# Optimization experiments

Hardware: AMD Instinct MI355X
Metric: run time of the kernel (lower is better)

## Reference

```python
import jax, jax.numpy as jnp
import numpy as np

QUALITY = 50

# standard JPEG luminance / chrominance quantization tables
_Y_TABLE = np.array([
    [16, 11, 10, 16, 24, 40, 51, 61],
    [12, 12, 14, 19, 26, 58, 60, 55],
    [14, 13, 16, 24, 40, 57, 69, 56],
    [14, 17, 22, 29, 51, 87, 80, 62],
    [18, 22, 37, 56, 68, 109, 103, 77],
    [24, 35, 55, 64, 81, 104, 113, 92],
    [49, 64, 78, 87, 103, 121, 120, 101],
    [72, 92, 95, 98, 112, 100, 103, 99]], dtype=np.float32)
_C_TABLE = np.full((8, 8), 99., dtype=np.float32)
_C_TABLE[:4, :4] = np.array([[17, 18, 24, 47], [18, 21, 26, 66],
                             [24, 26, 56, 99], [47, 66, 99, 99]], dtype=np.float32)

_i = np.arange(8)
_A = np.cos((2 * _i[:, None] + 1) * _i[None, :] * np.pi / 16).astype(np.float32)
_alpha = np.array([1.0 / np.sqrt(2)] + [1.0] * 7, dtype=np.float32)
_ALPHA2 = np.outer(_alpha, _alpha).astype(np.float32)        # idct pre-scale
_SCALE = (_ALPHA2 * 0.25).astype(np.float32)                 # dct post-scale

_RGB2YCC = np.array([[0.299, 0.587, 0.114],
                     [-0.168736, -0.331264, 0.5],
                     [0.5, -0.418688, -0.081312]], dtype=np.float32)
_SHIFT1 = np.array([0., 128., 128.], dtype=np.float32)
_YCC2RGB = np.array([[1., 0., 1.402],
                     [1., -0.344136, -0.714136],
                     [1., 1.772, 0.]], dtype=np.float32)
_SHIFT2 = np.array([0., -128., -128.], dtype=np.float32)


def _diff_round(x):
    r = jnp.round(x)
    return r + (x - r) ** 3


def _jpeg_channel(ch, table, factor):
    # ch: [B, h, w] -> blockwise DCT / quantize / dequant / IDCT -> [B, h, w]
    b, h, w = ch.shape
    blocks = ch.reshape(b, h // 8, 8, w // 8, 8).transpose(0, 1, 3, 2, 4).reshape(b, -1, 8, 8)
    A = jnp.asarray(_A)
    dct = jnp.asarray(_SCALE) * jnp.einsum('bnxy,xu,yv->bnuv', blocks - 128., A, A)
    qt = jnp.asarray(table) * factor
    q = _diff_round(dct / qt)
    deq = q * qt
    idct = 0.25 * jnp.einsum('bnuv,ux,vy->bnxy', deq * jnp.asarray(_ALPHA2), A, A) + 128.
    return idct.reshape(b, h // 8, w // 8, 8, 8).transpose(0, 1, 3, 2, 4).reshape(b, h, w)


def _diff_jpeg(x, quality):
    # quality -> scaling factor
    q = float(quality)
    factor = (5000. / q if q < 50 else 200. - 2. * q) / 100.
    x = jnp.clip(x, 0., 1.)
    img = jnp.transpose(x, (0, 2, 3, 1)) * 255.                      # [B,H,W,3]
    ycc = img @ jnp.asarray(_RGB2YCC).T + jnp.asarray(_SHIFT1)
    y, cb, cr = ycc[..., 0], ycc[..., 1], ycc[..., 2]
    b, h, w = y.shape
    # 4:2:0 chroma subsampling via 2x2 average pooling
    cb_s = cb.reshape(b, h // 2, 2, w // 2, 2).mean(axis=(2, 4))
    cr_s = cr.reshape(b, h // 2, 2, w // 2, 2).mean(axis=(2, 4))
    y2 = _jpeg_channel(y, _Y_TABLE, factor)
    cb2 = _jpeg_channel(cb_s, _C_TABLE, factor)
    cr2 = _jpeg_channel(cr_s, _C_TABLE, factor)
    cb_u = jnp.repeat(jnp.repeat(cb2, 2, axis=1), 2, axis=2)
    cr_u = jnp.repeat(jnp.repeat(cr2, 2, axis=1), 2, axis=2)
    ycc2 = jnp.stack([y2, cb_u, cr_u], axis=-1)
    rgb = (ycc2 + jnp.asarray(_SHIFT2)) @ jnp.asarray(_YCC2RGB).T
    rgb = jnp.clip(rgb, 0., 255.) / 255.
    out = jnp.transpose(rgb, (0, 3, 1, 2))                           # back to NCHW
    return jnp.clip(out, 0., 1.)


def setup_inputs() -> dict:
    key = jax.random.key(0)
    x = jax.random.uniform(key, (32, 3, 512, 512), dtype=jnp.float32)
    return {"x": x}


def reference(x):
    return _diff_jpeg(x, QUALITY)
```

## Files before the change

### kernel.cpp

```cpp
#include <hip/hip_runtime.h>
#include <math.h>

#define HH 512
#define WW 512

typedef float f2 __attribute__((ext_vector_type(2)));
typedef float f4 __attribute__((ext_vector_type(4)));

#define YS2  36
#define CS2  18
#define OY   0
#define OCB  576
#define OCR  720
#define OSCR 864
#define OAB  OSCR
#define WSZ  1272

static __device__ __forceinline__ f4 vclamp01x255(f4 v) {
    f4 z = 0.f, one = 1.f;
    return __builtin_elementwise_max(__builtin_elementwise_min(v, one), z) * 255.f;
}

__device__ __constant__ float YTAB[64] = {
    16,11,10,16,24,40,51,61,
    12,12,14,19,26,58,60,55,
    14,13,16,24,40,57,69,56,
    14,17,22,29,51,87,80,62,
    18,22,37,56,68,109,103,77,
    24,35,55,64,81,104,113,92,
    49,64,78,87,103,121,120,101,
    72,92,95,98,112,100,103,99};
__device__ __constant__ float CTAB[64] = {
    17,18,24,47,99,99,99,99,
    18,21,26,66,99,99,99,99,
    24,26,56,99,99,99,99,99,
    47,66,99,99,99,99,99,99,
    99,99,99,99,99,99,99,99,
    99,99,99,99,99,99,99,99,
    99,99,99,99,99,99,99,99,
    99,99,99,99,99,99,99,99};

__global__ __launch_bounds__(256) void jpeg_fused(const float* __restrict__ in,
                                                  float* __restrict__ out)
{
#pragma clang fp contract(off)
    __shared__ float Wall[4][WSZ];

    const int tid  = threadIdx.x;
    const int wid  = tid >> 6;
    const int lane = tid & 63;
    float* W = Wall[wid];

    const int wv    = blockIdx.x * 4 + wid;
    const int b     = wv >> 9;
    const int strip = (wv >> 4) & 31;
    const int pairc = wv & 15;
    const int h0    = strip * 16;
    const int w0    = pairc * 32;
    const size_t plane = (size_t)HH * WW;

    const int rp  = lane >> 3;
    const int pr  = rp * 2;
    const int c4  = (lane & 7) * 4;
    const size_t gbase = ((size_t)b * 3 * HH + (size_t)(h0 + pr)) * WW + (w0 + c4);

    f4 Lr0 = *(const f4*)(in + gbase);
    f4 Lr1 = *(const f4*)(in + gbase + WW);
    f4 Lg0 = *(const f4*)(in + gbase + plane);
    f4 Lg1 = *(const f4*)(in + gbase + plane + WW);
    f4 Lb0 = *(const f4*)(in + gbase + 2 * plane);
    f4 Lb1 = *(const f4*)(in + gbase + 2 * plane + WW);

    {
        int x = lane >> 3, u = lane & 7;
        double arg = (double)((2 * x + 1) * u) * 3.14159265358979323846 / 16.0;
        W[OAB + lane] = (float)cos(arg);
    }
    f2 As2[32];
#pragma unroll
    for (int k = 0; k < 32; ++k) {
        As2[k][0] = __int_as_float(__builtin_amdgcn_readfirstlane(__float_as_int(W[OAB + 2 * k])));
        As2[k][1] = __int_as_float(__builtin_amdgcn_readfirstlane(__float_as_int(W[OAB + 2 * k + 1])));
    }
    asm volatile("" ::: "memory");

    {
        f4 r0 = vclamp01x255(Lr0), r1 = vclamp01x255(Lr1);
        f4 g0 = vclamp01x255(Lg0), g1 = vclamp01x255(Lg1);
        f4 b0 = vclamp01x255(Lb0), b1 = vclamp01x255(Lb1);
        f4 y0  = ((r0 * 0.299f)     + (g0 * 0.587f))     + (b0 * 0.114f);
        f4 y1  = ((r1 * 0.299f)     + (g1 * 0.587f))     + (b1 * 0.114f);
        f4 cb0 = ((r0 * -0.168736f) + (g0 * -0.331264f)) + (b0 * 0.5f);
        f4 cb1 = ((r1 * -0.168736f) + (g1 * -0.331264f)) + (b1 * 0.5f);
        f4 cr0 = ((r0 * 0.5f)       + (g0 * -0.418688f)) + (b0 * -0.081312f);
        f4 cr1 = ((r1 * 0.5f)       + (g1 * -0.418688f)) + (b1 * -0.081312f);
        cb0 = cb0 + 128.f; cb1 = cb1 + 128.f;
        cr0 = cr0 + 128.f; cr1 = cr1 + 128.f;
        y0 = y0 - 128.f;  y1 = y1 - 128.f;
        *(f4*)&W[OY + pr * YS2 + c4]       = y0;
        *(f4*)&W[OY + (pr + 1) * YS2 + c4] = y1;
        f2 mb, mr;
        {
            float s01 = cb0.x + cb0.y, s23 = cb1.x + cb1.y;
            mb[0] = (s01 + s23) / 4.0f;
            float t01 = cb0.z + cb0.w, t23 = cb1.z + cb1.w;
            mb[1] = (t01 + t23) / 4.0f;
        }
        {
            float s01 = cr0.x + cr0.y, s23 = cr1.x + cr1.y;
            mr[0] = (s01 + s23) / 4.0f;
            float t01 = cr0.z + cr0.w, t23 = cr1.z + cr1.w;
            mr[1] = (t01 + t23) / 4.0f;
        }
        *(f2*)&W[OCB + rp * CS2 + (lane & 7) * 2] = mb;
        *(f2*)&W[OCR + rp * CS2 + (lane & 7) * 2] = mr;
    }
    asm volatile("" ::: "memory");

    const int g = lane >> 3, j = lane & 7;
#pragma unroll
    for (int pass = 0; pass < 2; ++pass) {
        if (g < 6) {
            const int it   = pass * 6 + g;
            const bool isY = (it < 8);
            float* scr = &W[OSCR + g * 68];

            float X[8];
            int by = 0, bx = 0, ob = 0;
            if (isY) {
                by = it >> 2; bx = it & 3;
#pragma unroll
                for (int x = 0; x < 8; ++x)
                    X[x] = W[OY + (by * 8 + x) * YS2 + bx * 8 + j];
            } else {
                ob = (it < 10) ? OCB : OCR;
                bx = (it < 10) ? (it - 8) : (it - 10);
#pragma unroll
                for (int x = 0; x < 8; ++x)
                    X[x] = W[ob + x * CS2 + bx * 8 + j] - 128.f;
            }

            f2 Tv[4];
#pragma unroll
            for (int m = 0; m < 4; ++m) {
                f2 a = {0.f, 0.f};
#pragma unroll
                for (int x = 0; x < 8; ++x) {
                    f2 xx = {X[x], X[x]};
                    a = __builtin_elementwise_fma(xx, As2[x * 4 + m], a);
                }
                Tv[m] = a;
            }
#pragma unroll
            for (int m = 0; m < 4; ++m) {
                scr[(2 * m) * 8 + j]     = Tv[m][0];
                scr[(2 * m + 1) * 8 + j] = Tv[m][1];
            }
            float Tt[8];
            {
                float4 a = *(const float4*)&scr[j * 8];
                float4 c = *(const float4*)&scr[j * 8 + 4];
                Tt[0] = a.x; Tt[1] = a.y; Tt[2] = a.z; Tt[3] = a.w;
                Tt[4] = c.x; Tt[5] = c.y; Tt[6] = c.z; Tt[7] = c.w;
            }
            float R[8];
#pragma unroll
            for (int m = 0; m < 4; ++m) {
                f2 a = {0.f, 0.f};
#pragma unroll
                for (int y = 0; y < 8; ++y) {
                    f2 tt = {Tt[y], Tt[y]};
                    a = __builtin_elementwise_fma(tt, As2[y * 4 + m], a);
                }
                R[2 * m] = a[0]; R[2 * m + 1] = a[1];
            }
            const float* QT = isY ? YTAB : CTAB;
            float qt[8];
            {
                float4 a = *(const float4*)&QT[j * 8];
                float4 c = *(const float4*)&QT[j * 8 + 4];
                qt[0] = a.x; qt[1] = a.y; qt[2] = a.z; qt[3] = a.w;
                qt[4] = c.x; qt[5] = c.y; qt[6] = c.z; qt[7] = c.w;
            }
            const float RC = 0.70710678118654752440f;
            float au = (j == 0) ? RC : 1.0f;
            float G[8];
#pragma unroll
            for (int v = 0; v < 8; ++v) {
                float av    = (v == 0) ? RC : 1.0f;
                float a2    = au * av;
                float scale = a2 * 0.25f;
                float dct   = scale * R[v];
                float xq    = dct / qt[v];
                float rd    = rintf(xq);
                float d     = xq - rd;
                float cube  = (d * d) * d;
                float qq    = rd + cube;
                float deq   = qq * qt[v];
                G[v] = deq * a2;
            }
#pragma unroll
            for (int v = 0; v < 8; ++v) scr[v * 8 + j] = G[v];
            float Gt[8];
            {
                float4 a = *(const float4*)&scr[j * 8];
                float4 c = *(const float4*)&scr[j * 8 + 4];
                Gt[0] = a.x; Gt[1] = a.y; Gt[2] = a.z; Gt[3] = a.w;
                Gt[4] = c.x; Gt[5] = c.y; Gt[6] = c.z; Gt[7] = c.w;
            }
            f2 T2v[4];
#pragma unroll
            for (int m = 0; m < 4; ++m) {
                f2 a = {0.f, 0.f};
#pragma unroll
                for (int u = 0; u < 8; ++u) {
                    f2 gg = {Gt[u], Gt[u]};
                    a = __builtin_elementwise_fma(gg, As2[u * 4 + m], a);
                }
                T2v[m] = a;
            }
#pragma unroll
            for (int m = 0; m < 4; ++m) {
                scr[(2 * m) * 8 + j]     = T2v[m][0];
                scr[(2 * m + 1) * 8 + j] = T2v[m][1];
            }
            float T2t[8];
            {
                float4 a = *(const float4*)&scr[j * 8];
                float4 c = *(const float4*)&scr[j * 8 + 4];
                T2t[0] = a.x; T2t[1] = a.y; T2t[2] = a.z; T2t[3] = a.w;
                T2t[4] = c.x; T2t[5] = c.y; T2t[6] = c.z; T2t[7] = c.w;
            }
            float O[8];
#pragma unroll
            for (int m = 0; m < 4; ++m) {
                f2 a = {0.f, 0.f};
#pragma unroll
                for (int v = 0; v < 8; ++v) {
                    f2 tt = {T2t[v], T2t[v]};
                    a = __builtin_elementwise_fma(tt, As2[v * 4 + m], a);
                }
                a = (a * 0.25f) + 128.f;
                O[2 * m] = a[0]; O[2 * m + 1] = a[1];
            }
            if (isY) {
                *(f4*)&W[OY + (by * 8 + j) * YS2 + bx * 8]     = (f4){O[0], O[1], O[2], O[3]};
                *(f4*)&W[OY + (by * 8 + j) * YS2 + bx * 8 + 4] = (f4){O[4], O[5], O[6], O[7]};
            } else {
                *(f4*)&W[ob + j * CS2 + bx * 8]     = (f4){O[0], O[1], O[2], O[3]};
                *(f4*)&W[ob + j * CS2 + bx * 8 + 4] = (f4){O[4], O[5], O[6], O[7]};
            }
        }
        asm volatile("" ::: "memory");
    }

    {
        const float INV255 = 1.0f / 255.0f;
        f4 ya = *(const f4*)&W[OY + pr * YS2 + c4];
        f4 yb = *(const f4*)&W[OY + (pr + 1) * YS2 + c4];
        f2 cbp = *(const f2*)&W[OCB + rp * CS2 + (lane & 7) * 2];
        f2 crp = *(const f2*)&W[OCR + rp * CS2 + (lane & 7) * 2];
        float cb0 = cbp[0] - 128.f, cb1 = cbp[1] - 128.f;
        float cr0 = crp[0] - 128.f, cr1 = crp[1] - 128.f;
        f4 cbm = {cb0, cb0, cb1, cb1};
        f4 crm = {cr0, cr0, cr1, cr1};
        f4 z = 0.f, m255 = 255.f;
#pragma unroll
        for (int row = 0; row < 2; ++row) {
            f4 yy = row ? yb : ya;
            f4 rv = yy + (crm * 1.402f);
            f4 gv = (yy + (cbm * -0.344136f)) + (crm * -0.714136f);
            f4 bv = yy + (cbm * 1.772f);
            rv = __builtin_elementwise_max(__builtin_elementwise_min(rv, m255), z) * INV255;
            gv = __builtin_elementwise_max(__builtin_elementwise_min(gv, m255), z) * INV255;
            bv = __builtin_elementwise_max(__builtin_elementwise_min(bv, m255), z) * INV255;
            size_t base = gbase + (size_t)row * WW;
            __builtin_nontemporal_store(rv, (f4*)(out + base));
            __builtin_nontemporal_store(gv, (f4*)(out + base + plane));
            __builtin_nontemporal_store(bv, (f4*)(out + base + 2 * plane));
        }
    }
}

extern "C" void kernel_launch(void* const* d_in, const int* in_sizes, int n_in,
                              void* d_out, int out_size, void* d_ws, size_t ws_size,
                              hipStream_t stream)
{
    const float* x = (const float*)d_in[0];
    float* o = (float*)d_out;
    int batch  = in_sizes[0] / (3 * HH * WW);
    int blocks = batch * 512 / 4;
    jpeg_fused<<<blocks, 256, 0, stream>>>(x, o);
}
```

Measured before the change: 40.68 us.

## Process two tiles per wave with prefetch of second tile during DCT

Each wave now handles two adjacent 32-column tiles instead of one, halving the grid. The second tile's global loads are issued before the first tile's DCT work so memory latency overlaps with compute. The cosine-table setup is also amortised over two tiles. The trade-offs are higher register pressure from holding the prefetched tile and fewer waves available to hide latency.

```diff
diff --git a/kernel.cpp b/kernel.cpp
--- a/kernel.cpp
+++ b/kernel.cpp
@@ -52,42 +52,37 @@
     float* W = Wall[wid];
 
     const int wv    = blockIdx.x * 4 + wid;
-    const int b     = wv >> 9;
-    const int strip = (wv >> 4) & 31;
-    const int pairc = wv & 15;
+    const int b     = wv >> 8;
+    const int strip = (wv >> 3) & 31;
+    const int seg   = wv & 7;
     const int h0    = strip * 16;
-    const int w0    = pairc * 32;
+    const int w0    = seg * 64;
     const size_t plane = (size_t)HH * WW;
 
     const int rp  = lane >> 3;
     const int pr  = rp * 2;
     const int c4  = (lane & 7) * 4;
-    const size_t gbase = ((size_t)b * 3 * HH + (size_t)(h0 + pr)) * WW + (w0 + c4);
-
-    f4 Lr0 = *(const f4*)(in + gbase);
-    f4 Lr1 = *(const f4*)(in + gbase + WW);
-    f4 Lg0 = *(const f4*)(in + gbase + plane);
-    f4 Lg1 = *(const f4*)(in + gbase + plane + WW);
-    f4 Lb0 = *(const f4*)(in + gbase + 2 * plane);
-    f4 Lb1 = *(const f4*)(in + gbase + 2 * plane + WW);
-
-    {
-        int x = lane >> 3, u = lane & 7;
-        double arg = (double)((2 * x + 1) * u) * 3.14159265358979323846 / 16.0;
-        W[OAB + lane] = (float)cos(arg);
-    }
+    const size_t grow   = ((size_t)b * 3 * HH + (size_t)(h0 + pr)) * WW + c4;
+    const size_t gbase0 = grow + w0;
+    const size_t gbase1 = grow + w0 + 32;
+
+    const int g = lane >> 3, j = lane & 7;
     f2 As2[32];
-#pragma unroll
-    for (int k = 0; k < 32; ++k) {
-        As2[k][0] = __int_as_float(__builtin_amdgcn_readfirstlane(__float_as_int(W[OAB + 2 * k])));
-        As2[k][1] = __int_as_float(__builtin_amdgcn_readfirstlane(__float_as_int(W[OAB + 2 * k + 1])));
-    }
-    asm volatile("" ::: "memory");
-
-    {
-        f4 r0 = vclamp01x255(Lr0), r1 = vclamp01x255(Lr1);
-        f4 g0 = vclamp01x255(Lg0), g1 = vclamp01x255(Lg1);
-        f4 b0 = vclamp01x255(Lb0), b1 = vclamp01x255(Lb1);
+
+    auto loadT = [&](f4* L, size_t gb) {
+        L[0] = *(const f4*)(in + gb);
+        L[1] = *(const f4*)(in + gb + WW);
+        L[2] = *(const f4*)(in + gb + plane);
+        L[3] = *(const f4*)(in + gb + plane + WW);
+        L[4] = *(const f4*)(in + gb + 2 * plane);
+        L[5] = *(const f4*)(in + gb + 2 * plane + WW);
+    };
+
+    auto stageT = [&](const f4* L) {
+#pragma clang fp contract(off)
+        f4 r0 = vclamp01x255(L[0]), r1 = vclamp01x255(L[1]);
+        f4 g0 = vclamp01x255(L[2]), g1 = vclamp01x255(L[3]);
+        f4 b0 = vclamp01x255(L[4]), b1 = vclamp01x255(L[5]);
         f4 y0  = ((r0 * 0.299f)     + (g0 * 0.587f))     + (b0 * 0.114f);
         f4 y1  = ((r1 * 0.299f)     + (g1 * 0.587f))     + (b1 * 0.114f);
         f4 cb0 = ((r0 * -0.168736f) + (g0 * -0.331264f)) + (b0 * 0.5f);
@@ -114,147 +109,149 @@
         }
         *(f2*)&W[OCB + rp * CS2 + (lane & 7) * 2] = mb;
         *(f2*)&W[OCR + rp * CS2 + (lane & 7) * 2] = mr;
-    }
-    asm volatile("" ::: "memory");
-
-    const int g = lane >> 3, j = lane & 7;
-#pragma unroll
-    for (int pass = 0; pass < 2; ++pass) {
-        if (g < 6) {
-            const int it   = pass * 6 + g;
-            const bool isY = (it < 8);
-            float* scr = &W[OSCR + g * 68];
-
-            float X[8];
-            int by = 0, bx = 0, ob = 0;
-            if (isY) {
-                by = it >> 2; bx = it & 3;
-#pragma unroll
-                for (int x = 0; x < 8; ++x)
-                    X[x] = W[OY + (by * 8 + x) * YS2 + bx * 8 + j];
-            } else {
-                ob = (it < 10) ? OCB : OCR;
-                bx = (it < 10) ? (it - 8) : (it - 10);
-#pragma unroll
-                for (int x = 0; x < 8; ++x)
-                    X[x] = W[ob + x * CS2 + bx * 8 + j] - 128.f;
+    };
+
+    auto dctAll = [&]() {
+#pragma clang fp contract(off)
+#pragma unroll
+        for (int pass = 0; pass < 2; ++pass) {
+            if (g < 6) {
+                const int it   = pass * 6 + g;
+                const bool isY = (it < 8);
+                float* scr = &W[OSCR + g * 68];
+
+                float X[8];
+                int by = 0, bx = 0, ob = 0;
+                if (isY) {
+                    by = it >> 2; bx = it & 3;
+#pragma unroll
+                    for (int x = 0; x < 8; ++x)
+                        X[x] = W[OY + (by * 8 + x) * YS2 + bx * 8 + j];
+                } else {
+                    ob = (it < 10) ? OCB : OCR;
+                    bx = (it < 10) ? (it - 8) : (it - 10);
+#pragma unroll
+                    for (int x = 0; x < 8; ++x)
+                        X[x] = W[ob + x * CS2 + bx * 8 + j] - 128.f;
+                }
+
+                f2 Tv[4];
+#pragma unroll
+                for (int m = 0; m < 4; ++m) {
+                    f2 a = {0.f, 0.f};
+#pragma unroll
+                    for (int x = 0; x < 8; ++x) {
+                        f2 xx = {X[x], X[x]};
+                        a = __builtin_elementwise_fma(xx, As2[x * 4 + m], a);
+                    }
+                    Tv[m] = a;
+                }
+#pragma unroll
+                for (int m = 0; m < 4; ++m) {
+                    scr[(2 * m) * 8 + j]     = Tv[m][0];
+                    scr[(2 * m + 1) * 8 + j] = Tv[m][1];
+                }
+                float Tt[8];
+                {
+                    float4 a = *(const float4*)&scr[j * 8];
+                    float4 c = *(const float4*)&scr[j * 8 + 4];
+                    Tt[0] = a.x; Tt[1] = a.y; Tt[2] = a.z; Tt[3] = a.w;
+                    Tt[4] = c.x; Tt[5] = c.y; Tt[6] = c.z; Tt[7] = c.w;
+                }
+                float R[8];
+#pragma unroll
+                for (int m = 0; m < 4; ++m) {
+                    f2 a = {0.f, 0.f};
+#pragma unroll
+                    for (int y = 0; y < 8; ++y) {
+                        f2 tt = {Tt[y], Tt[y]};
+                        a = __builtin_elementwise_fma(tt, As2[y * 4 + m], a);
+                    }
+                    R[2 * m] = a[0]; R[2 * m + 1] = a[1];
+                }
+                const float* QT = isY ? YTAB : CTAB;
+                float qt[8];
+                {
+                    float4 a = *(const float4*)&QT[j * 8];
+                    float4 c = *(const float4*)&QT[j * 8 + 4];
+                    qt[0] = a.x; qt[1] = a.y; qt[2] = a.z; qt[3] = a.w;
+                    qt[4] = c.x; qt[5] = c.y; qt[6] = c.z; qt[7] = c.w;
+                }
+                const float RC = 0.70710678118654752440f;
+                float au = (j == 0) ? RC : 1.0f;
+                float G[8];
+#pragma unroll
+                for (int v = 0; v < 8; ++v) {
+                    float av    = (v == 0) ? RC : 1.0f;
+                    float a2    = au * av;
+                    float scale = a2 * 0.25f;
+                    float dct   = scale * R[v];
+                    float xq    = dct / qt[v];
+                    float rd    = rintf(xq);
+                    float d     = xq - rd;
+                    float cube  = (d * d) * d;
+                    float qq    = rd + cube;
+                    float deq   = qq * qt[v];
+                    G[v] = deq * a2;
+                }
+#pragma unroll
+                for (int v = 0; v < 8; ++v) scr[v * 8 + j] = G[v];
+                float Gt[8];
+                {
+                    float4 a = *(const float4*)&scr[j * 8];
+                    float4 c = *(const float4*)&scr[j * 8 + 4];
+                    Gt[0] = a.x; Gt[1] = a.y; Gt[2] = a.z; Gt[3] = a.w;
+                    Gt[4] = c.x; Gt[5] = c.y; Gt[6] = c.z; Gt[7] = c.w;
+                }
+                f2 T2v[4];
+#pragma unroll
+                for (int m = 0; m < 4; ++m) {
+                    f2 a = {0.f, 0.f};
+#pragma unroll
+                    for (int u = 0; u < 8; ++u) {
+                        f2 gg = {Gt[u], Gt[u]};
+                        a = __builtin_elementwise_fma(gg, As2[u * 4 + m], a);
+                    }
+                    T2v[m] = a;
+                }
+#pragma unroll
+                for (int m = 0; m < 4; ++m) {
+                    scr[(2 * m) * 8 + j]     = T2v[m][0];
+                    scr[(2 * m + 1) * 8 + j] = T2v[m][1];
+                }
+                float T2t[8];
+                {
+                    float4 a = *(const float4*)&scr[j * 8];
+                    float4 c = *(const float4*)&scr[j * 8 + 4];
+                    T2t[0] = a.x; T2t[1] = a.y; T2t[2] = a.z; T2t[3] = a.w;
+                    T2t[4] = c.x; T2t[5] = c.y; T2t[6] = c.z; T2t[7] = c.w;
+                }
+                float O[8];
+#pragma unroll
+                for (int m = 0; m < 4; ++m) {
+                    f2 a = {0.f, 0.f};
+#pragma unroll
+                    for (int v = 0; v < 8; ++v) {
+                        f2 tt = {T2t[v], T2t[v]};
+                        a = __builtin_elementwise_fma(tt, As2[v * 4 + m], a);
+                    }
+                    a = (a * 0.25f) + 128.f;
+                    O[2 * m] = a[0]; O[2 * m + 1] = a[1];
+                }
+                if (isY) {
+                    *(f4*)&W[OY + (by * 8 + j) * YS2 + bx * 8]     = (f4){O[0], O[1], O[2], O[3]};
+                    *(f4*)&W[OY + (by * 8 + j) * YS2 + bx * 8 + 4] = (f4){O[4], O[5], O[6], O[7]};
+                } else {
+                    *(f4*)&W[ob + j * CS2 + bx * 8]     = (f4){O[0], O[1], O[2], O[3]};
+                    *(f4*)&W[ob + j * CS2 + bx * 8 + 4] = (f4){O[4], O[5], O[6], O[7]};
+                }
             }
-
-            f2 Tv[4];
-#pragma unroll
-            for (int m = 0; m < 4; ++m) {
-                f2 a = {0.f, 0.f};
-#pragma unroll
-                for (int x = 0; x < 8; ++x) {
-                    f2 xx = {X[x], X[x]};
-                    a = __builtin_elementwise_fma(xx, As2[x * 4 + m], a);
-                }
-                Tv[m] = a;
-            }
-#pragma unroll
-            for (int m = 0; m < 4; ++m) {
-                scr[(2 * m) * 8 + j]     = Tv[m][0];
-                scr[(2 * m + 1) * 8 + j] = Tv[m][1];
-            }
-            float Tt[8];
-            {
-                float4 a = *(const float4*)&scr[j * 8];
-                float4 c = *(const float4*)&scr[j * 8 + 4];
-                Tt[0] = a.x; Tt[1] = a.y; Tt[2] = a.z; Tt[3] = a.w;
-                Tt[4] = c.x; Tt[5] = c.y; Tt[6] = c.z; Tt[7] = c.w;
-            }
-            float R[8];
-#pragma unroll
-            for (int m = 0; m < 4; ++m) {
-                f2 a = {0.f, 0.f};
-#pragma unroll
-                for (int y = 0; y < 8; ++y) {
-                    f2 tt = {Tt[y], Tt[y]};
-                    a = __builtin_elementwise_fma(tt, As2[y * 4 + m], a);
-                }
-                R[2 * m] = a[0]; R[2 * m + 1] = a[1];
-            }
-            const float* QT = isY ? YTAB : CTAB;
-            float qt[8];
-            {
-                float4 a = *(const float4*)&QT[j * 8];
-                float4 c = *(const float4*)&QT[j * 8 + 4];
-                qt[0] = a.x; qt[1] = a.y; qt[2] = a.z; qt[3] = a.w;
-                qt[4] = c.x; qt[5] = c.y; qt[6] = c.z; qt[7] = c.w;
-            }
-            const float RC = 0.70710678118654752440f;
-            float au = (j == 0) ? RC : 1.0f;
-            float G[8];
-#pragma unroll
-            for (int v = 0; v < 8; ++v) {
-                float av    = (v == 0) ? RC : 1.0f;
-                float a2    = au * av;
-                float scale = a2 * 0.25f;
-                float dct   = scale * R[v];
-                float xq    = dct / qt[v];
-                float rd    = rintf(xq);
-                float d     = xq - rd;
-                float cube  = (d * d) * d;
-                float qq    = rd + cube;
-                float deq   = qq * qt[v];
-                G[v] = deq * a2;
-            }
-#pragma unroll
-            for (int v = 0; v < 8; ++v) scr[v * 8 + j] = G[v];
-            float Gt[8];
-            {
-                float4 a = *(const float4*)&scr[j * 8];
-                float4 c = *(const float4*)&scr[j * 8 + 4];
-                Gt[0] = a.x; Gt[1] = a.y; Gt[2] = a.z; Gt[3] = a.w;
-                Gt[4] = c.x; Gt[5] = c.y; Gt[6] = c.z; Gt[7] = c.w;
-            }
-            f2 T2v[4];
-#pragma unroll
-            for (int m = 0; m < 4; ++m) {
-                f2 a = {0.f, 0.f};
-#pragma unroll
-                for (int u = 0; u < 8; ++u) {
-                    f2 gg = {Gt[u], Gt[u]};
-                    a = __builtin_elementwise_fma(gg, As2[u * 4 + m], a);
-                }
-                T2v[m] = a;
-            }
-#pragma unroll
-            for (int m = 0; m < 4; ++m) {
-                scr[(2 * m) * 8 + j]     = T2v[m][0];
-                scr[(2 * m + 1) * 8 + j] = T2v[m][1];
-            }
-            float T2t[8];
-            {
-                float4 a = *(const float4*)&scr[j * 8];
-                float4 c = *(const float4*)&scr[j * 8 + 4];
-                T2t[0] = a.x; T2t[1] = a.y; T2t[2] = a.z; T2t[3] = a.w;
-                T2t[4] = c.x; T2t[5] = c.y; T2t[6] = c.z; T2t[7] = c.w;
-            }
-            float O[8];
-#pragma unroll
-            for (int m = 0; m < 4; ++m) {
-                f2 a = {0.f, 0.f};
-#pragma unroll
-                for (int v = 0; v < 8; ++v) {
-                    f2 tt = {T2t[v], T2t[v]};
-                    a = __builtin_elementwise_fma(tt, As2[v * 4 + m], a);
-                }
-                a = (a * 0.25f) + 128.f;
-                O[2 * m] = a[0]; O[2 * m + 1] = a[1];
-            }
-            if (isY) {
-                *(f4*)&W[OY + (by * 8 + j) * YS2 + bx * 8]     = (f4){O[0], O[1], O[2], O[3]};
-                *(f4*)&W[OY + (by * 8 + j) * YS2 + bx * 8 + 4] = (f4){O[4], O[5], O[6], O[7]};
-            } else {
-                *(f4*)&W[ob + j * CS2 + bx * 8]     = (f4){O[0], O[1], O[2], O[3]};
-                *(f4*)&W[ob + j * CS2 + bx * 8 + 4] = (f4){O[4], O[5], O[6], O[7]};
-            }
+            asm volatile("" ::: "memory");
         }
-        asm volatile("" ::: "memory");
-    }
-
-    {
+    };
+
+    auto outputT = [&](size_t gb) {
+#pragma clang fp contract(off)
         const float INV255 = 1.0f / 255.0f;
         f4 ya = *(const f4*)&W[OY + pr * YS2 + c4];
         f4 yb = *(const f4*)&W[OY + (pr + 1) * YS2 + c4];
@@ -274,12 +271,38 @@
             rv = __builtin_elementwise_max(__builtin_elementwise_min(rv, m255), z) * INV255;
             gv = __builtin_elementwise_max(__builtin_elementwise_min(gv, m255), z) * INV255;
             bv = __builtin_elementwise_max(__builtin_elementwise_min(bv, m255), z) * INV255;
-            size_t base = gbase + (size_t)row * WW;
+            size_t base = gb + (size_t)row * WW;
             __builtin_nontemporal_store(rv, (f4*)(out + base));
             __builtin_nontemporal_store(gv, (f4*)(out + base + plane));
             __builtin_nontemporal_store(bv, (f4*)(out + base + 2 * plane));
         }
+    };
+
+    f4 L1[6], L2[6];
+    loadT(L1, gbase0);
+
+    {
+        int x = lane >> 3, u = lane & 7;
+        double arg = (double)((2 * x + 1) * u) * 3.14159265358979323846 / 16.0;
+        W[OAB + lane] = (float)cos(arg);
     }
+#pragma unroll
+    for (int k = 0; k < 32; ++k) {
+        As2[k][0] = __int_as_float(__builtin_amdgcn_readfirstlane(__float_as_int(W[OAB + 2 * k])));
+        As2[k][1] = __int_as_float(__builtin_amdgcn_readfirstlane(__float_as_int(W[OAB + 2 * k + 1])));
+    }
+    asm volatile("" ::: "memory");
+
+    stageT(L1);
+    loadT(L2, gbase1);
+    asm volatile("" ::: "memory");
+    dctAll();
+    outputT(gbase0);
+    asm volatile("" ::: "memory");
+    stageT(L2);
+    asm volatile("" ::: "memory");
+    dctAll();
+    outputT(gbase1);
 }
 
 extern "C" void kernel_launch(void* const* d_in, const int* in_sizes, int n_in,
@@ -289,6 +312,6 @@
     const float* x = (const float*)d_in[0];
     float* o = (float*)d_out;
     int batch  = in_sizes[0] / (3 * HH * WW);
-    int blocks = batch * 512 / 4;
+    int blocks = batch * 256 / 4;
     jpeg_fused<<<blocks, 256, 0, stream>>>(x, o);
 }
```

Measured after the change: 41.00 us. No clear change (+0.8%).
